# Kernel optimization log

Measured on AMD Instinct MI355X. Metric: run time of the kernel, lower is better.

## Reference

```python
import jax, jax.numpy as jnp
import numpy as np

B = 8192
D = 512          # encode_length
H = 1024         # projection hidden
S = 4096         # fine_Nums (fine prototypes)
Y = 256          # coarse_num
GUMBEL_TEMP = 0.5
EPS_LOG = 1e-9
EPS_GUMBEL = 1e-20


def setup_inputs() -> dict:
    key = jax.random.key(0)
    ks = jax.random.split(key, 16)
    g = lambda k, shape, s: jax.random.normal(k, shape, dtype=jnp.float32) * s
    glorot = lambda k, shape: jax.random.uniform(k, shape, dtype=jnp.float32,
                                                 minval=-1.0, maxval=1.0) * jnp.sqrt(6.0 / (shape[0] + shape[1]))
    return {
        "X": jax.random.normal(ks[0], (B, D), dtype=jnp.float32),
        # projectionHead: Linear(D,H) -> ReLU -> Linear(H,D)
        "W1": g(ks[1], (D, H), 0.05), "b1": jnp.zeros((H,), jnp.float32),
        "W2": g(ks[2], (H, D), 0.05), "b2": jnp.zeros((D,), jnp.float32),
        # sigma_head: Linear(D,H) -> ReLU -> Linear(H,D)
        "Ws1": g(ks[3], (D, H), 0.05), "bs1": jnp.zeros((H,), jnp.float32),
        "Ws2": g(ks[4], (H, D), 0.05), "bs2": jnp.zeros((D,), jnp.float32),
        # prototype codebooks (glorot)
        "mu_y": glorot(ks[5], (Y, D)),
        "mu_s": glorot(ks[6], (S, D)),
        # reparameterization + gumbel noise (explicit for determinism)
        "eps": jax.random.normal(ks[7], (B, D), dtype=jnp.float32),
        "u_s": jax.random.uniform(ks[8], (B, S), dtype=jnp.float32),
        "u_y": jax.random.uniform(ks[9], (B, Y), dtype=jnp.float32),
    }


def _neg_sq_dist(x, c):
    # -||x_i - c_j||^2 computed via expansion (same math as (x-c)**2 sum)
    return -(jnp.sum(x * x, -1, keepdims=True)
             - 2.0 * x @ c.T
             + jnp.sum(c * c, -1)[None, :])


def _gumbel_softmax_soft(logits_original, u, temp):
    # torch: logits = log(softmax(logits_original) + 1e-9); y = softmax((logits + g)/temp)
    logits = jnp.log(jax.nn.softmax(logits_original, axis=-1) + EPS_LOG)
    gnoise = -jnp.log(-jnp.log(u + EPS_GUMBEL) + EPS_GUMBEL)
    return jax.nn.softmax((logits + gnoise) / temp, axis=-1)


def reference(X, W1, b1, W2, b2, Ws1, bs1, Ws2, bs2, mu_y, mu_s, eps, u_s, u_y):
    # VAE encode with reparameterization
    mu = jax.nn.relu(X @ W1 + b1) @ W2 + b2                    # [B, D]
    sigma = jax.nn.softplus(jax.nn.relu(X @ Ws1 + bs1) @ Ws2 + bs2)
    Z = mu + sigma * eps                                       # [B, D]

    # fine prototype routing: cdist + gumbel-softmax + hard assign
    logits_s = _neg_sq_dist(Z, mu_s)                            # [B, S]
    soft_prob = _gumbel_softmax_soft(logits_s, u_s, GUMBEL_TEMP)
    fine_idx = jnp.argmax(soft_prob, axis=1)                    # [B]
    hard_prob = jax.nn.one_hot(fine_idx, S, dtype=jnp.float32)  # [B, S]
    z_q = hard_prob @ mu_s                                      # selected fine proto [B, D]

    # coarse routing conditioned on Z and selected fine prototype
    logits_coarse = 0.5 * (_neg_sq_dist(Z, mu_y) + _neg_sq_dist(z_q, mu_y))  # [B, Y]
    soft_prob_y = _gumbel_softmax_soft(logits_coarse, u_y, GUMBEL_TEMP)
    batch_y = jnp.argmax(soft_prob_y, axis=1)                   # [B] int

    return mu, Z, soft_prob, soft_prob_y, hard_prob, batch_y
```

## Files before the change

kernel.cpp:

```cpp
#include <hip/hip_runtime.h>
#include <hip/hip_bf16.h>

#define B_ 8192
#define D_ 512
#define H_ 1024
#define S_ 4096
#define Y_ 256

constexpr size_t O_MU    = 0;
constexpr size_t O_Z     = (size_t)B_ * D_;
constexpr size_t O_SOFT  = O_Z + (size_t)B_ * D_;
constexpr size_t O_SOFTY = O_SOFT + (size_t)B_ * S_;
constexpr size_t O_HARD  = O_SOFTY + (size_t)B_ * Y_;
constexpr size_t O_BY    = O_HARD + (size_t)B_ * S_;

typedef _Float16 half8 __attribute__((ext_vector_type(8)));
typedef float f32x4 __attribute__((ext_vector_type(4)));
typedef unsigned int u32;

__device__ __forceinline__ void gload16(const void* g, void* l) {
  __builtin_amdgcn_global_load_lds((const __attribute__((address_space(1))) u32*)g,
                                   (__attribute__((address_space(3))) u32*)l,
                                   16, 0, 0);
}

__device__ __forceinline__ void split2(float x, _Float16& h, _Float16& l) {
  _Float16 hi = (_Float16)x;
  h = hi;
  l = (_Float16)((x - (float)hi) * 2048.0f);
}

__device__ __forceinline__ float blockMax(float v, float* sh) {
#pragma unroll
  for (int o = 32; o; o >>= 1) v = fmaxf(v, __shfl_xor(v, o));
  if ((threadIdx.x & 63) == 0) sh[threadIdx.x >> 6] = v;
  __syncthreads();
  float r = fmaxf(fmaxf(sh[0], sh[1]), fmaxf(sh[2], sh[3]));
  __syncthreads();
  return r;
}

__device__ __forceinline__ float blockSum(float v, float* sh) {
#pragma unroll
  for (int o = 32; o; o >>= 1) v += __shfl_xor(v, o);
  if ((threadIdx.x & 63) == 0) sh[threadIdx.x >> 6] = v;
  __syncthreads();
  float r = (sh[0] + sh[1]) + (sh[2] + sh[3]);
  __syncthreads();
  return r;
}

__device__ __forceinline__ void blockArgmax(float& v, int& i, float* shf, int* shi) {
#pragma unroll
  for (int o = 32; o; o >>= 1) {
    float v2 = __shfl_xor(v, o);
    int   i2 = __shfl_xor(i, o);
    if (v2 > v || (v2 == v && i2 < i)) { v = v2; i = i2; }
  }
  if ((threadIdx.x & 63) == 0) { shf[threadIdx.x >> 6] = v; shi[threadIdx.x >> 6] = i; }
  __syncthreads();
  float bv = shf[0]; int bi = shi[0];
#pragma unroll
  for (int k = 1; k < 4; ++k) {
    float v2 = shf[k]; int i2 = shi[k];
    if (v2 > bv || (v2 == bv && i2 < bi)) { bv = v2; bi = i2; }
  }
  v = bv; i = bi;
  __syncthreads();
}

__device__ void seg_split(const float* __restrict__ s, _Float16* __restrict__ h,
                          _Float16* __restrict__ l, size_t n, int b, int nb) {
  size_t i = (size_t)b * 256 + threadIdx.x;
  size_t st = (size_t)nb * 256;
  for (; i < n; i += st) { _Float16 hi, lo; split2(s[i], hi, lo); h[i] = hi; l[i] = lo; }
}

__device__ void seg_tsplit(const float* __restrict__ W, int K, int N,
                           _Float16* __restrict__ th, _Float16* __restrict__ tl,
                           int tile, float (*tl_lds)[33]) {
  int ntn = N / 32;
  int nb = (tile % ntn) * 32, kb = (tile / ntn) * 32;
  int tx = threadIdx.x & 31, ty = threadIdx.x >> 5;
  for (int r = ty; r < 32; r += 8)
    tl_lds[r][tx] = W[(size_t)(kb + r) * N + nb + tx];
  __syncthreads();
  for (int r = ty; r < 32; r += 8) {
    float x = tl_lds[tx][r];
    size_t o = (size_t)(nb + r) * K + kb + tx;
    _Float16 hi, lo; split2(x, hi, lo);
    th[o] = hi; tl[o] = lo;
  }
}

__device__ void seg_rownorm(const float* __restrict__ A, int K, float* __restrict__ out,
                            int tile) {
  int w = threadIdx.x >> 6, lane = threadIdx.x & 63;
  int row = tile * 4 + w;
  const float* a = A + (size_t)row * K;
  float s = 0.f;
  for (int k = lane; k < K; k += 64) { float x = a[k]; s += x * x; }
#pragma unroll
  for (int o = 32; o; o >>= 1) s += __shfl_xor(s, o);
  if (lane == 0) out[row] = s;
}

__global__ __launch_bounds__(256) void prep_kernel(
    const float* __restrict__ X, const float* __restrict__ W1, const float* __restrict__ Ws1,
    const float* __restrict__ W2, const float* __restrict__ Ws2,
    const float* __restrict__ mu_s, const float* __restrict__ mu_y,
    _Float16* XH, _Float16* XL, _Float16* MSH, _Float16* MSL,
    _Float16* MYH, _Float16* MYL,
    _Float16* W1CH, _Float16* W1CL, _Float16* W2CH, _Float16* W2CL,
    float* CS2, float* CY2) {
  __shared__ float tile[32][33];
  int b = blockIdx.x;
  if (b < 512)       seg_split(X,    XH,  XL,  (size_t)B_ * D_, b,        512);
  else if (b < 768)  seg_split(mu_s, MSH, MSL, (size_t)S_ * D_, b - 512,  256);
  else if (b < 784)  seg_split(mu_y, MYH, MYL, (size_t)Y_ * D_, b - 768,  16);
  else if (b < 1296) seg_tsplit(W1,  D_, H_, W1CH, W1CL, b - 784, tile);
  else if (b < 1808) seg_tsplit(Ws1, D_, H_, W1CH + (size_t)H_ * D_,
                                W1CL + (size_t)H_ * D_, b - 1296, tile);
  else if (b < 2320) seg_tsplit(W2,  H_, D_, W2CH, W2CL, b - 1808, tile);
  else if (b < 2832) seg_tsplit(Ws2, H_, D_, W2CH + (size_t)D_ * H_,
                                W2CL + (size_t)D_ * H_, b - 2320, tile);
  else if (b < 3856) seg_rownorm(mu_s, D_, CS2, b - 2832);
  else               seg_rownorm(mu_y, D_, CY2, b - 3856);
}

template <int EPI>
__launch_bounds__(256, 2)
__global__ void gemm_split(const _Float16* __restrict__ Ah, const _Float16* __restrict__ Al,
                           const _Float16* __restrict__ Bh, const _Float16* __restrict__ Bl,
                           int N, int K, int lda, int ldc, int nsplit, int aoff2,
                           const float* __restrict__ bias, const float* __restrict__ bias2,
                           float* __restrict__ Cf,
                           _Float16* __restrict__ Ch, _Float16* __restrict__ Cl,
                           const float* __restrict__ rown, const float* __restrict__ coln) {
  __shared__ _Float16 lds[4 * 8192];
  const int tid = threadIdx.x;
  const int w = tid >> 6, lane = tid & 63;
  const int m0 = blockIdx.y * 128, n0 = blockIdx.x * 128;
  const int g4 = lane >> 4, l15 = lane & 15;
  const int ln3 = lane >> 3, l7 = lane & 7;
  const int wsx = l7 ^ ln3;
  const int strideA = (w < 2) ? lda : K;
  const size_t laneoff = (size_t)ln3 * strideA + (size_t)wsx * 8;
  const int ashift = (n0 >= nsplit) ? aoff2 : 0;

  const _Float16* stage_src =
      (w == 0) ? (Ah + (size_t)m0 * lda + ashift) :
      (w == 1) ? (Al + (size_t)m0 * lda + ashift) :
      (w == 2) ? (Bh + (size_t)n0 * K) : (Bl + (size_t)n0 * K);
  _Float16* stage_dst = &lds[w * 8192];

  const int wm = w >> 1, wn = w & 1;

  f32x4 acc[4][4] = {};
  f32x4 accc[4][4] = {};

  for (int k0 = 0; k0 < K; k0 += 64) {
    const _Float16* sp = stage_src + k0 + laneoff;
#pragma unroll
    for (int q = 0; q < 16; ++q)
      gload16(sp + (size_t)q * 8 * strideA, stage_dst + q * 512);
    __syncthreads();

#pragma unroll
    for (int kk = 0; kk < 2; ++kk) {
      half8 ah[4], al[4], bh[4], bl[4];
#pragma unroll
      for (int mi = 0; mi < 4; ++mi) {
        int row = wm * 64 + mi * 16 + l15;
        int off = row * 64 + (((kk * 4 + g4) ^ (l15 & 7)) * 8);
        ah[mi] = *(const half8*)&lds[off];
        al[mi] = *(const half8*)&lds[8192 + off];
      }
#pragma unroll
      for (int ni = 0; ni < 4; ++ni) {
        int row = wn * 64 + ni * 16 + l15;
        int off = row * 64 + (((kk * 4 + g4) ^ (l15 & 7)) * 8);
        bh[ni] = *(const half8*)&lds[16384 + off];
        bl[ni] = *(const half8*)&lds[24576 + off];
      }
#pragma unroll
      for (int mi = 0; mi < 4; ++mi)
#pragma unroll
        for (int ni = 0; ni < 4; ++ni) {
          acc[mi][ni]  = __builtin_amdgcn_mfma_f32_16x16x32_f16(ah[mi], bh[ni], acc[mi][ni], 0, 0, 0);
          accc[mi][ni] = __builtin_amdgcn_mfma_f32_16x16x32_f16(ah[mi], bl[ni], accc[mi][ni], 0, 0, 0);
          accc[mi][ni] = __builtin_amdgcn_mfma_f32_16x16x32_f16(al[mi], bh[ni], accc[mi][ni], 0, 0, 0);
        }
    }
    __syncthreads();
  }

#pragma unroll
  for (int mi = 0; mi < 4; ++mi)
#pragma unroll
    for (int ni = 0; ni < 4; ++ni)
#pragma unroll
      for (int r = 0; r < 4; ++r) {
        int m = m0 + wm * 64 + mi * 16 + g4 * 4 + r;
        int n = n0 + wn * 64 + ni * 16 + l15;
        float c = acc[mi][ni][r] + accc[mi][ni][r] * (1.0f / 2048.0f);
        size_t idx = (size_t)m * ldc + n;
        if (EPI == 0) {
          float bv = (n < nsplit) ? bias[n] : bias2[n - nsplit];
          c = fmaxf(c + bv, 0.0f);
          _Float16 hi, lo; split2(c, hi, lo);
          Ch[idx] = hi; Cl[idx] = lo;
        } else if (EPI == 1) {
          float bv = (n < nsplit) ? bias[n] : bias2[n - nsplit];
          Cf[idx] = c + bv;
        } else {
          Cf[idx] = 2.0f * c - rown[m] - coln[n];
        }
      }
}

__global__ __launch_bounds__(256) void kz_kernel(const float* __restrict__ MPS,
                                                 const float* __restrict__ eps,
                                                 float* __restrict__ out,
                                                 _Float16* __restrict__ Zh,
                                                 _Float16* __restrict__ Zl,
                                                 float* __restrict__ z2) {
  __shared__ float sh[4];
  int row = blockIdx.x, t = threadIdx.x;
  float s = 0.f;
  for (int j = t; j < D_; j += 256) {
    size_t idx = (size_t)row * D_ + j;
    float m = MPS[(size_t)row * 1024 + j];
    float p = MPS[(size_t)row * 1024 + 512 + j];
    float e = eps[idx];
    float sp = fmaxf(p, 0.f) + log1pf(expf(-fabsf(p)));
    float z = m + sp * e;
    out[O_MU + idx] = m;
    out[O_Z + idx] = z;
    _Float16 hi, lo; split2(z, hi, lo);
    Zh[idx] = hi; Zl[idx] = lo;
    s += z * z;
  }
#pragma unroll
  for (int o = 32; o; o >>= 1) s += __shfl_xor(s, o);
  if ((t & 63) == 0) sh[t >> 6] = s;
  __syncthreads();
  if (t == 0) z2[row] = (sh[0] + sh[1]) + (sh[2] + sh[3]);
}

__global__ __launch_bounds__(256) void ks_kernel(const float* __restrict__ logits,
                                                 const float* __restrict__ us,
                                                 float* __restrict__ out,
                                                 int* __restrict__ fidx, int row0) {
  __shared__ float shf[4];
  __shared__ int shi[4];
  int row = row0 + blockIdx.x, t = threadIdx.x;
  const float4* l4 = (const float4*)(logits + (size_t)blockIdx.x * S_) + t * 4;
  const float4* u4 = (const float4*)(us + (size_t)row * S_) + t * 4;

  float v[16];
#pragma unroll
  for (int q = 0; q < 4; ++q) {
    float4 x = l4[q];
    v[q * 4 + 0] = x.x; v[q * 4 + 1] = x.y; v[q * 4 + 2] = x.z; v[q * 4 + 3] = x.w;
  }
  float m1 = -3.4e38f;
#pragma unroll
  for (int k = 0; k < 16; ++k) m1 = fmaxf(m1, v[k]);
  m1 = blockMax(m1, shf);
  float s1 = 0.f;
#pragma unroll
  for (int k = 0; k < 16; ++k) { v[k] = __expf(v[k] - m1); s1 += v[k]; }
  s1 = blockSum(s1, shf);
  float is1 = 1.0f / s1;
  float m2 = -3.4e38f;
#pragma unroll
  for (int q = 0; q < 4; ++q) {
    float4 uu = u4[q];
    float ua[4] = {uu.x, uu.y, uu.z, uu.w};
#pragma unroll
    for (int e = 0; e < 4; ++e) {
      int k = q * 4 + e;
      float p = v[k] * is1 + 1e-9f;
      float g = -logf(-logf(ua[e] + 1e-20f) + 1e-20f);
      v[k] = (logf(p) + g) * 2.0f;
      m2 = fmaxf(m2, v[k]);
    }
  }
  m2 = blockMax(m2, shf);
  float s2 = 0.f;
#pragma unroll
  for (int k = 0; k < 16; ++k) { v[k] = __expf(v[k] - m2); s2 += v[k]; }
  s2 = blockSum(s2, shf);
  float is2 = 1.0f / s2;
  float bv = -3.4e38f; int bi = 0x7fffffff;
  float* so = out + O_SOFT + (size_t)row * S_ + (size_t)t * 16;
#pragma unroll
  for (int q = 0; q < 4; ++q) {
    float pe[4];
#pragma unroll
    for (int e = 0; e < 4; ++e) {
      int k = q * 4 + e;
      pe[e] = v[k] * is2;
      if (pe[e] > bv) { bv = pe[e]; bi = t * 16 + k; }
    }
    float4 pv; pv.x = pe[0]; pv.y = pe[1]; pv.z = pe[2]; pv.w = pe[3];
    ((float4*)so)[q] = pv;
  }
  blockArgmax(bv, bi, shf, shi);
  float* ho = out + O_HARD + (size_t)row * S_ + (size_t)t * 16;
#pragma unroll
  for (int q = 0; q < 4; ++q) {
    float4 hv;
    hv.x = (t * 16 + q * 4 + 0 == bi) ? 1.f : 0.f;
    hv.y = (t * 16 + q * 4 + 1 == bi) ? 1.f : 0.f;
    hv.z = (t * 16 + q * 4 + 2 == bi) ? 1.f : 0.f;
    hv.w = (t * 16 + q * 4 + 3 == bi) ? 1.f : 0.f;
    ((float4*)ho)[q] = hv;
  }
  if (t == 0) fidx[row] = bi;
}

__global__ __launch_bounds__(256) void ky_kernel(const float* __restrict__ lzy,
                                                 const float* __restrict__ lsy,
                                                 const int* __restrict__ fidx,
                                                 const float* __restrict__ uy,
                                                 float* __restrict__ out) {
  __shared__ float shf[4];
  __shared__ int shi[4];
  int row = blockIdx.x, t = threadIdx.x;
  int fi = fidx[row];
  float lc = 0.5f * (lzy[(size_t)row * Y_ + t] + lsy[(size_t)fi * Y_ + t]);
  float m1 = blockMax(lc, shf);
  float e = __expf(lc - m1);
  float s1 = blockSum(e, shf);
  float p = e / s1 + 1e-9f;
  float g = -logf(-logf(uy[(size_t)row * Y_ + t] + 1e-20f) + 1e-20f);
  float a = (logf(p) + g) * 2.0f;
  float m2 = blockMax(a, shf);
  float y = __expf(a - m2);
  float s2 = blockSum(y, shf);
  float sp = y / s2;
  out[O_SOFTY + (size_t)row * Y_ + t] = sp;
  float bv = sp; int bi = t;
  blockArgmax(bv, bi, shf, shi);
  if (t == 0) out[O_BY + row] = (float)bi;
}

extern "C" void kernel_launch(void* const* d_in, const int* in_sizes, int n_in,
                              void* d_out, int out_size, void* d_ws, size_t ws_size,
                              hipStream_t stream) {
  const float* X    = (const float*)d_in[0];
  const float* W1   = (const float*)d_in[1];
  const float* b1   = (const float*)d_in[2];
  const float* W2   = (const float*)d_in[3];
  const float* b2   = (const float*)d_in[4];
  const float* Ws1  = (const float*)d_in[5];
  const float* bs1  = (const float*)d_in[6];
  const float* Ws2  = (const float*)d_in[7];
  const float* bs2  = (const float*)d_in[8];
  const float* mu_y = (const float*)d_in[9];
  const float* mu_s = (const float*)d_in[10];
  const float* eps  = (const float*)d_in[11];
  const float* u_s  = (const float*)d_in[12];
  const float* u_y  = (const float*)d_in[13];
  float* out = (float*)d_out;

  char* ws = (char*)d_ws;
  _Float16* XH    = (_Float16*)(ws + 0);
  _Float16* XL    = (_Float16*)(ws + 8388608);
  _Float16* W1CH  = (_Float16*)(ws + 16777216);
  _Float16* W1CL  = (_Float16*)(ws + 18874368);
  _Float16* W2CH  = (_Float16*)(ws + 20971520);
  _Float16* W2CL  = (_Float16*)(ws + 23068672);
  _Float16* H1H   = (_Float16*)(ws + 25165824);
  _Float16* H1L   = (_Float16*)(ws + 58720256);
  float*    MPS   = (float*)  (ws + 92274688);
  float*    LOGH  = (float*)  (ws + 0);
  float*    LZY   = (float*)  (ws + 67108864);
  float*    LSY   = (float*)  (ws + 75497472);
  const size_t RB = 125829120;
  _Float16* MSH  = (_Float16*)(ws + RB + 0);
  _Float16* MSL  = (_Float16*)(ws + RB + 4194304);
  _Float16* MYH  = (_Float16*)(ws + RB + 8388608);
  _Float16* MYL  = (_Float16*)(ws + RB + 8650752);
  _Float16* ZH   = (_Float16*)(ws + RB + 8912896);
  _Float16* ZL   = (_Float16*)(ws + RB + 17301504);
  float*    Z2   = (float*)  (ws + RB + 25690112);
  float*    CS2  = (float*)  (ws + RB + 25722880);
  float*    CY2  = (float*)  (ws + RB + 25739264);
  int*      FIDX = (int*)    (ws + RB + 25743360);
  (void)ws_size; (void)in_sizes; (void)n_in; (void)out_size;

  prep_kernel<<<3920, 256, 0, stream>>>(X, W1, Ws1, W2, Ws2, mu_s, mu_y,
                                        XH, XL, MSH, MSL, MYH, MYL,
                                        W1CH, W1CL, W2CH, W2CL, CS2, CY2);

  gemm_split<0><<<dim3(2 * H_ / 128, B_ / 128), 256, 0, stream>>>(
      XH, XL, W1CH, W1CL, 2 * H_, D_, D_, 2 * H_, H_, 0,
      b1, bs1, nullptr, H1H, H1L, nullptr, nullptr);

  gemm_split<1><<<dim3(2 * D_ / 128, B_ / 128), 256, 0, stream>>>(
      H1H, H1L, W2CH, W2CL, 2 * D_, H_, 2 * H_, 2 * D_, D_, H_,
      b2, bs2, MPS, nullptr, nullptr, nullptr, nullptr);

  kz_kernel<<<B_, 256, 0, stream>>>(MPS, eps, out, ZH, ZL, Z2);

  gemm_split<2><<<dim3(S_ / 128, 4096 / 128), 256, 0, stream>>>(
      ZH, ZL, MSH, MSL, S_, D_, D_, S_, S_, 0,
      nullptr, nullptr, LOGH, nullptr, nullptr, Z2, CS2);
  ks_kernel<<<4096, 256, 0, stream>>>(LOGH, u_s, out, FIDX, 0);
  gemm_split<2><<<dim3(S_ / 128, 4096 / 128), 256, 0, stream>>>(
      ZH + (size_t)4096 * D_, ZL + (size_t)4096 * D_, MSH, MSL, S_, D_, D_, S_, S_, 0,
      nullptr, nullptr, LOGH, nullptr, nullptr, Z2 + 4096, CS2);
  ks_kernel<<<4096, 256, 0, stream>>>(LOGH, u_s, out, FIDX, 4096);

  gemm_split<2><<<dim3(Y_ / 128, B_ / 128), 256, 0, stream>>>(
      ZH, ZL, MYH, MYL, Y_, D_, D_, Y_, Y_, 0,
      nullptr, nullptr, LZY, nullptr, nullptr, Z2, CY2);
  gemm_split<2><<<dim3(Y_ / 128, S_ / 128), 256, 0, stream>>>(
      MSH, MSL, MYH, MYL, Y_, D_, D_, Y_, Y_, 0,
      nullptr, nullptr, LSY, nullptr, nullptr, CS2, CY2);
  ky_kernel<<<B_, 256, 0, stream>>>(LZY, LSY, FIDX, u_y, out);
}
```

Measured before the change: 418.4 us.

## Fuse coarse routing into fine softmax kernel and merge prototype GEMM launches

The fine-prototype logits are now written directly into the soft_prob output region by a single full-batch GEMM, which the softmax kernel then overwrites in place. The two coarse-distance GEMMs are merged into one launch by laying out Z/mu_s halves and their norm arrays contiguously. The coarse gumbel-softmax is fused into the fine routing kernel, using the argmax index directly instead of a FIDX round trip. This cuts kernel launches and intermediate workspace traffic, but relies on careful workspace layout and an in-place read-then-write of the output buffer.

```diff
diff --git a/kernel.cpp b/kernel.cpp
--- a/kernel.cpp
+++ b/kernel.cpp
@@ -248,14 +248,15 @@
   if (t == 0) z2[row] = (sh[0] + sh[1]) + (sh[2] + sh[3]);
 }
 
-__global__ __launch_bounds__(256) void ks_kernel(const float* __restrict__ logits,
-                                                 const float* __restrict__ us,
-                                                 float* __restrict__ out,
-                                                 int* __restrict__ fidx, int row0) {
+__global__ __launch_bounds__(256) void ks_kernel(const float* __restrict__ us,
+                                                 const float* __restrict__ lzy,
+                                                 const float* __restrict__ lsy,
+                                                 const float* __restrict__ uy,
+                                                 float* __restrict__ out) {
   __shared__ float shf[4];
   __shared__ int shi[4];
-  int row = row0 + blockIdx.x, t = threadIdx.x;
-  const float4* l4 = (const float4*)(logits + (size_t)blockIdx.x * S_) + t * 4;
+  int row = blockIdx.x, t = threadIdx.x;
+  const float4* l4 = (const float4*)(out + O_SOFT + (size_t)row * S_) + t * 4;
   const float4* u4 = (const float4*)(us + (size_t)row * S_) + t * 4;
 
   float v[16];
@@ -318,33 +319,22 @@
     hv.w = (t * 16 + q * 4 + 3 == bi) ? 1.f : 0.f;
     ((float4*)ho)[q] = hv;
   }
-  if (t == 0) fidx[row] = bi;
-}
-
-__global__ __launch_bounds__(256) void ky_kernel(const float* __restrict__ lzy,
-                                                 const float* __restrict__ lsy,
-                                                 const int* __restrict__ fidx,
-                                                 const float* __restrict__ uy,
-                                                 float* __restrict__ out) {
-  __shared__ float shf[4];
-  __shared__ int shi[4];
-  int row = blockIdx.x, t = threadIdx.x;
-  int fi = fidx[row];
-  float lc = 0.5f * (lzy[(size_t)row * Y_ + t] + lsy[(size_t)fi * Y_ + t]);
-  float m1 = blockMax(lc, shf);
-  float e = __expf(lc - m1);
-  float s1 = blockSum(e, shf);
-  float p = e / s1 + 1e-9f;
-  float g = -logf(-logf(uy[(size_t)row * Y_ + t] + 1e-20f) + 1e-20f);
-  float a = (logf(p) + g) * 2.0f;
-  float m2 = blockMax(a, shf);
-  float y = __expf(a - m2);
-  float s2 = blockSum(y, shf);
-  float sp = y / s2;
-  out[O_SOFTY + (size_t)row * Y_ + t] = sp;
-  float bv = sp; int bi = t;
-  blockArgmax(bv, bi, shf, shi);
-  if (t == 0) out[O_BY + row] = (float)bi;
+
+  float lc = 0.5f * (lzy[(size_t)row * Y_ + t] + lsy[(size_t)bi * Y_ + t]);
+  float cm1 = blockMax(lc, shf);
+  float ce = __expf(lc - cm1);
+  float cs1 = blockSum(ce, shf);
+  float cp = ce / cs1 + 1e-9f;
+  float cg = -logf(-logf(uy[(size_t)row * Y_ + t] + 1e-20f) + 1e-20f);
+  float ca = (logf(cp) + cg) * 2.0f;
+  float cm2 = blockMax(ca, shf);
+  float cy = __expf(ca - cm2);
+  float cs2 = blockSum(cy, shf);
+  float csp = cy / cs2;
+  out[O_SOFTY + (size_t)row * Y_ + t] = csp;
+  float cbv = csp; int cbi = t;
+  blockArgmax(cbv, cbi, shf, shi);
+  if (t == 0) out[O_BY + row] = (float)cbi;
 }
 
 extern "C" void kernel_launch(void* const* d_in, const int* in_sizes, int n_in,
@@ -376,21 +366,21 @@
   _Float16* H1H   = (_Float16*)(ws + 25165824);
   _Float16* H1L   = (_Float16*)(ws + 58720256);
   float*    MPS   = (float*)  (ws + 92274688);
-  float*    LOGH  = (float*)  (ws + 0);
-  float*    LZY   = (float*)  (ws + 67108864);
-  float*    LSY   = (float*)  (ws + 75497472);
+  float*    LZY   = (float*)  (ws + 0);
+  float*    LSY   = (float*)  (ws + 8388608);
   const size_t RB = 125829120;
-  _Float16* MSH  = (_Float16*)(ws + RB + 0);
-  _Float16* MSL  = (_Float16*)(ws + RB + 4194304);
-  _Float16* MYH  = (_Float16*)(ws + RB + 8388608);
-  _Float16* MYL  = (_Float16*)(ws + RB + 8650752);
-  _Float16* ZH   = (_Float16*)(ws + RB + 8912896);
-  _Float16* ZL   = (_Float16*)(ws + RB + 17301504);
+  _Float16* ZH   = (_Float16*)(ws + RB + 0);
+  _Float16* MSH  = (_Float16*)(ws + RB + 8388608);
+  _Float16* ZL   = (_Float16*)(ws + RB + 12582912);
+  _Float16* MSL  = (_Float16*)(ws + RB + 20971520);
+  _Float16* MYH  = (_Float16*)(ws + RB + 25165824);
+  _Float16* MYL  = (_Float16*)(ws + RB + 25427968);
   float*    Z2   = (float*)  (ws + RB + 25690112);
   float*    CS2  = (float*)  (ws + RB + 25722880);
   float*    CY2  = (float*)  (ws + RB + 25739264);
-  int*      FIDX = (int*)    (ws + RB + 25743360);
   (void)ws_size; (void)in_sizes; (void)n_in; (void)out_size;
+
+  float* LOGITS = out + O_SOFT;
 
   prep_kernel<<<3920, 256, 0, stream>>>(X, W1, Ws1, W2, Ws2, mu_s, mu_y,
                                         XH, XL, MSH, MSL, MYH, MYL,
@@ -406,20 +396,13 @@
 
   kz_kernel<<<B_, 256, 0, stream>>>(MPS, eps, out, ZH, ZL, Z2);
 
-  gemm_split<2><<<dim3(S_ / 128, 4096 / 128), 256, 0, stream>>>(
+  gemm_split<2><<<dim3(S_ / 128, B_ / 128), 256, 0, stream>>>(
       ZH, ZL, MSH, MSL, S_, D_, D_, S_, S_, 0,
-      nullptr, nullptr, LOGH, nullptr, nullptr, Z2, CS2);
-  ks_kernel<<<4096, 256, 0, stream>>>(LOGH, u_s, out, FIDX, 0);
-  gemm_split<2><<<dim3(S_ / 128, 4096 / 128), 256, 0, stream>>>(
-      ZH + (size_t)4096 * D_, ZL + (size_t)4096 * D_, MSH, MSL, S_, D_, D_, S_, S_, 0,
-      nullptr, nullptr, LOGH, nullptr, nullptr, Z2 + 4096, CS2);
-  ks_kernel<<<4096, 256, 0, stream>>>(LOGH, u_s, out, FIDX, 4096);
-
-  gemm_split<2><<<dim3(Y_ / 128, B_ / 128), 256, 0, stream>>>(
+      nullptr, nullptr, LOGITS, nullptr, nullptr, Z2, CS2);
+
+  gemm_split<2><<<dim3(Y_ / 128, (B_ + S_) / 128), 256, 0, stream>>>(
       ZH, ZL, MYH, MYL, Y_, D_, D_, Y_, Y_, 0,
       nullptr, nullptr, LZY, nullptr, nullptr, Z2, CY2);
-  gemm_split<2><<<dim3(Y_ / 128, S_ / 128), 256, 0, stream>>>(
-      MSH, MSL, MYH, MYL, Y_, D_, D_, Y_, Y_, 0,
-      nullptr, nullptr, LSY, nullptr, nullptr, CS2, CY2);
-  ky_kernel<<<B_, 256, 0, stream>>>(LZY, LSY, FIDX, u_y, out);
-}
+
+  ks_kernel<<<B_, 256, 0, stream>>>(u_s, LZY, LSY, u_y, out);
+}
```

Result: faster. 376.9 us (-9.9%).
